# Optimization experiments

Measured on AMD Instinct MI355X. Metric: run time of the kernel, lower is better.

## Reference

```python
import jax, jax.numpy as jnp
import numpy as np

B, K, H, W = 8, 32, 480, 480
N, D = 576, 1024
NUM_CLASSES, CLS_DIM, OUT = 150, 64, 256
IN_DIM = D + CLS_DIM + 5


def setup_inputs() -> dict:
    key = jax.random.key(0)
    ks = jax.random.split(key, 8)
    return {
        "feature_map": jax.random.normal(ks[0], (B, N, D), dtype=jnp.float32),
        "masks": jax.random.randint(ks[1], (B, K, H, W), 0, 2, dtype=jnp.int32),
        "class_ids": jax.random.randint(ks[2], (B, K), 0, NUM_CLASSES, dtype=jnp.int64),
        "embed_table": jax.random.normal(ks[3], (NUM_CLASSES, CLS_DIM), dtype=jnp.float32),
        "W1": jax.random.normal(ks[4], (IN_DIM, OUT), dtype=jnp.float32) * 0.02,
        "b1": jnp.zeros((OUT,), dtype=jnp.float32),
        "ln_g": jnp.ones((OUT,), dtype=jnp.float32),
        "ln_b": jnp.zeros((OUT,), dtype=jnp.float32),
        "W2": jax.random.normal(ks[5], (OUT, OUT), dtype=jnp.float32) * 0.02,
        "b2": jnp.zeros((OUT,), dtype=jnp.float32),
    }


def _geom_feats(m):
    # m: [B,K,H,W] float binary masks -> [B,K,5] (cx, cy, area_norm, bbox_w, bbox_h)
    dt = m.dtype
    area = m.sum((-2, -1))                      # [B,K]
    safe = jnp.maximum(area, 1.0)
    xs = jnp.arange(W, dtype=dt)
    ys = jnp.arange(H, dtype=dt)
    cx = jnp.einsum('bkhw,w->bk', m, xs) / safe / W
    cy = jnp.einsum('bkhw,h->bk', m, ys) / safe / H
    col = m.max(axis=2)                          # [B,K,W] column occupancy
    row = m.max(axis=3)                          # [B,K,H] row occupancy
    x_min = jnp.min(jnp.where(col > 0, xs, float(W)), axis=-1)
    x_max = jnp.max(jnp.where(col > 0, xs, -1.0), axis=-1)
    y_min = jnp.min(jnp.where(row > 0, ys, float(H)), axis=-1)
    y_max = jnp.max(jnp.where(row > 0, ys, -1.0), axis=-1)
    bbox_w = (x_max - x_min + 1.0) / W
    bbox_h = (y_max - y_min + 1.0) / H
    area_norm = area / (H * W)
    geom = jnp.stack([cx, cy, area_norm, bbox_w, bbox_h], axis=-1)  # [B,K,5]
    valid = (area >= 1.0)[..., None]
    return jnp.where(valid, geom, 0.0)


def reference(feature_map, masks, class_ids, embed_table, W1, b1, ln_g, ln_b, W2, b2):
    Hf = Wf = int(round(N ** 0.5))  # 24
    m = (masks > 0).astype(feature_map.dtype)           # [B,K,H,W]
    # nearest-neighbor downsample (PyTorch 'nearest': src = floor(dst*in/out))
    idx_h = (jnp.arange(Hf) * H) // Hf
    idx_w = (jnp.arange(Wf) * W) // Wf
    m_rs = m[:, :, idx_h][:, :, :, idx_w]               # [B,K,Hf,Wf]
    m_flat = m_rs.reshape(B, K, Hf * Wf)                # [B,K,N]
    msum = jnp.clip(m_flat.sum(-1, keepdims=True), 1e-6, None)
    pooled = jnp.einsum('bkn,bnd->bkd', m_flat, feature_map) / msum  # [B,K,D]
    geom = _geom_feats(m)                               # [B,K,5]
    cls_emb = embed_table[class_ids]                    # [B,K,CLS_DIM]
    x = jnp.concatenate([pooled, cls_emb, geom], axis=-1)  # [B,K,IN_DIM]
    h = jax.nn.gelu(x @ W1 + b1, approximate=False)
    mu = h.mean(-1, keepdims=True)
    var = jnp.mean((h - mu) ** 2, axis=-1, keepdims=True)
    hn = (h - mu) * jax.lax.rsqrt(var + 1e-5) * ln_g + ln_b
    return hn @ W2 + b2                                 # [B,K,OUT]
```

## Files before the change

### kernel.cpp

```cpp
#include <hip/hip_runtime.h>
#include <math.h>

#define Bb 8
#define Kk 32
#define Hh 480
#define Ww 480
#define Nn 576
#define Dd 1024
#define CLSD 64
#define OUTD 256
#define INDIM 1093
#define BK 256
#define PIX4 57600

#define DS_OFF   0
#define META_OFF 147456

__global__ __launch_bounds__(1024) void kA(const int* __restrict__ masks,
                                           float* __restrict__ ws) {
  const int bk = blockIdx.x;
  const int t  = threadIdx.x;
  const int4* mp = (const int4*)(masks + (size_t)bk * (Hh * Ww));

  __shared__ float ds[576];
  __shared__ int s_area, s_sumx, s_sumy, s_cnt;
  __shared__ int s_minx, s_maxx, s_miny, s_maxy;
  if (t == 0) {
    s_area = 0; s_sumx = 0; s_sumy = 0; s_cnt = 0;
    s_minx = Ww; s_maxx = -1; s_miny = Hh; s_maxy = -1;
  }
  __syncthreads();

  int area = 0, sumx = 0, sumy = 0, cntds = 0;
  int minx = Ww, maxx = -1, miny = Hh, maxy = -1;

  auto body = [&](int q, int4 v) {
    int h   = q / 120;
    int rem = q - h * 120;
    int w0  = rem * 4;
    int m0 = v.x > 0, m1 = v.y > 0, m2 = v.z > 0, m3 = v.w > 0;
    int c = m0 + m1 + m2 + m3;
    area += c;
    sumy += h * c;
    sumx += w0 * c + m1 + 2 * m2 + 3 * m3;
    if (c) {
      miny = min(miny, h);
      maxy = max(maxy, h);
      int lo = m0 ? w0 : (m1 ? w0 + 1 : (m2 ? w0 + 2 : w0 + 3));
      int hi = m3 ? w0 + 3 : (m2 ? w0 + 2 : (m1 ? w0 + 1 : w0));
      minx = min(minx, lo);
      maxx = max(maxx, hi);
    }
    int a20 = h / 20;
    int c5  = rem / 5;
    if (h == a20 * 20 && rem == c5 * 5) {
      ds[a20 * 24 + c5] = (float)m0;
      cntds += m0;
    }
  };

#pragma unroll 4
  for (int i = 0; i < 56; i++) {
    int q = t + (i << 10);
    body(q, mp[q]);
  }
  if (t < 256) {
    int q = 57344 + t;
    body(q, mp[q]);
  }

  for (int off = 32; off; off >>= 1) {
    area  += __shfl_down(area, off);
    sumx  += __shfl_down(sumx, off);
    sumy  += __shfl_down(sumy, off);
    cntds += __shfl_down(cntds, off);
    minx = min(minx, __shfl_down(minx, off));
    maxx = max(maxx, __shfl_down(maxx, off));
    miny = min(miny, __shfl_down(miny, off));
    maxy = max(maxy, __shfl_down(maxy, off));
  }
  if ((t & 63) == 0) {
    atomicAdd(&s_area, area);
    atomicAdd(&s_sumx, sumx);
    atomicAdd(&s_sumy, sumy);
    atomicAdd(&s_cnt, cntds);
    atomicMin(&s_minx, minx);
    atomicMax(&s_maxx, maxx);
    atomicMin(&s_miny, miny);
    atomicMax(&s_maxy, maxy);
  }
  __syncthreads();

  float* ws_ds = ws + DS_OFF + (size_t)bk * 576;
  if (t < 576) ws_ds[t] = ds[t];

  if (t == 0) {
    float* meta = ws + META_OFF + (size_t)bk * 8;
    float areaf = (float)s_area;
    float safe  = fmaxf(areaf, 1.0f);
    float cx = ((float)s_sumx / safe) * (1.0f / Ww);
    float cy = ((float)s_sumy / safe) * (1.0f / Hh);
    float an = areaf * (1.0f / (Hh * Ww));
    float bw = (float)(s_maxx - s_minx + 1) * (1.0f / Ww);
    float bh = (float)(s_maxy - s_miny + 1) * (1.0f / Hh);
    if (s_area < 1) { cx = 0.f; cy = 0.f; an = 0.f; bw = 0.f; bh = 0.f; }
    meta[0] = cx; meta[1] = cy; meta[2] = an; meta[3] = bw; meta[4] = bh;
    meta[5] = 1.0f / fmaxf((float)s_cnt, 1e-6f);
    meta[6] = (float)s_cnt;
  }
}

__global__ __launch_bounds__(256) void kBC(const float* __restrict__ fm,
                                           const int* __restrict__ cids,
                                           const float* __restrict__ emb,
                                           const float* __restrict__ W1,
                                           const float* __restrict__ b1,
                                           const float* __restrict__ lg,
                                           const float* __restrict__ lb,
                                           const float* __restrict__ W2,
                                           const float* __restrict__ b2,
                                           const float* __restrict__ ws,
                                           float* __restrict__ out) {
  const int b    = blockIdx.x & 7;
  const int k    = blockIdx.x >> 3;
  const int bk   = b * Kk + k;
  const int t    = threadIdx.x;
  const int lane = t & 63;
  const int w    = t >> 6;

  __shared__ float4 x4s[292];
  __shared__ int   act[576];
  __shared__ int   nact;
  __shared__ float partial[4 * 256];
  __shared__ float hrow[256];
  __shared__ float red[8];
  float* x = (float*)x4s;

  if (t == 0) nact = 0;
  __syncthreads();

  const float* dsrow = ws + DS_OFF + (size_t)bk * 576;
  for (int i = t; i < 576; i += 256) {
    float mv = dsrow[i];
    if (mv != 0.0f) act[atomicAdd(&nact, 1)] = i;
  }
  if (t < 75) x[1093 + t] = 0.0f;
  __syncthreads();
  const int na = nact;

  const float* meta = ws + META_OFF + (size_t)bk * 8;
  float inv = meta[5];
  float ax = 0.f, ay = 0.f, az = 0.f, aw = 0.f;
  const float4* fmp = (const float4*)fm + (size_t)b * Nn * (Dd / 4);
  int j = 0;
  for (; j + 4 <= na; j += 4) {
    int4 nn = *(const int4*)(act + j);
    float4 f0 = fmp[nn.x * (Dd / 4) + t];
    float4 f1 = fmp[nn.y * (Dd / 4) + t];
    float4 f2 = fmp[nn.z * (Dd / 4) + t];
    float4 f3 = fmp[nn.w * (Dd / 4) + t];
    ax += f0.x + f1.x + f2.x + f3.x;
    ay += f0.y + f1.y + f2.y + f3.y;
    az += f0.z + f1.z + f2.z + f3.z;
    aw += f0.w + f1.w + f2.w + f3.w;
  }
  for (; j < na; j++) {
    float4 f = fmp[act[j] * (Dd / 4) + t];
    ax += f.x; ay += f.y; az += f.z; aw += f.w;
  }
  float4 p;
  p.x = ax * inv; p.y = ay * inv; p.z = az * inv; p.w = aw * inv;
  x4s[t] = p;
  if (t < CLSD) x[Dd + t] = emb[(size_t)cids[bk] * CLSD + t];
  else if (t < CLSD + 5) x[Dd + t] = meta[t - CLSD];
  __syncthreads();

  const int kbeg = w * 292;
  const int kend = min(INDIM, kbeg + 292);
  float acc0 = 0.f, acc1 = 0.f, acc2 = 0.f, acc3 = 0.f;
  int kk = kbeg;
  for (; kk + 4 <= kend; kk += 4) {
    float4 xv = x4s[kk >> 2];
    const float* xs = (const float*)&xv;
#pragma unroll
    for (int u = 0; u < 4; u++) {
      float xval = xs[u];
      const float* wrow = W1 + (size_t)(kk + u) * OUTD;
      acc0 = fmaf(xval, wrow[lane], acc0);
      acc1 = fmaf(xval, wrow[lane + 64], acc1);
      acc2 = fmaf(xval, wrow[lane + 128], acc2);
      acc3 = fmaf(xval, wrow[lane + 192], acc3);
    }
  }
  for (; kk < kend; kk++) {
    float xval = x[kk];
    const float* wrow = W1 + (size_t)kk * OUTD;
    acc0 = fmaf(xval, wrow[lane], acc0);
    acc1 = fmaf(xval, wrow[lane + 64], acc1);
    acc2 = fmaf(xval, wrow[lane + 128], acc2);
    acc3 = fmaf(xval, wrow[lane + 192], acc3);
  }
  partial[w * 256 + lane] = acc0;
  partial[w * 256 + lane + 64] = acc1;
  partial[w * 256 + lane + 128] = acc2;
  partial[w * 256 + lane + 192] = acc3;
  __syncthreads();

  float hval = partial[t] + partial[256 + t] + partial[512 + t] + partial[768 + t] + b1[t];
  hval = 0.5f * hval * (1.0f + erff(hval * 0.7071067811865475f));
  float s = hval, q = hval * hval;
  for (int off = 32; off; off >>= 1) {
    s += __shfl_down(s, off);
    q += __shfl_down(q, off);
  }
  if (lane == 0) { red[w] = s; red[4 + w] = q; }
  __syncthreads();
  float mu  = (red[0] + red[1] + red[2] + red[3]) * (1.0f / OUTD);
  float var = (red[4] + red[5] + red[6] + red[7]) * (1.0f / OUTD) - mu * mu;
  float ist = 1.0f / sqrtf(var + 1e-5f);
  float hn  = (hval - mu) * ist * lg[t] + lb[t];
  hrow[t] = hn;
  __syncthreads();

  float c = b2[t];
  const float4* h4 = (const float4*)hrow;
  for (int i = 0; i < 64; i++) {
    float4 hv = h4[i];
    const float* hs = (const float*)&hv;
#pragma unroll
    for (int u = 0; u < 4; u++)
      c = fmaf(hs[u], W2[(size_t)(i * 4 + u) * OUTD + t], c);
  }
  out[(size_t)bk * OUTD + t] = c;
}

extern "C" void kernel_launch(void* const* d_in, const int* in_sizes, int n_in,
                              void* d_out, int out_size, void* d_ws, size_t ws_size,
                              hipStream_t stream) {
  const float* fm    = (const float*)d_in[0];
  const int*   masks = (const int*)d_in[1];
  const int*   cids  = (const int*)d_in[2];
  const float* emb   = (const float*)d_in[3];
  const float* W1    = (const float*)d_in[4];
  const float* b1    = (const float*)d_in[5];
  const float* lg    = (const float*)d_in[6];
  const float* lb    = (const float*)d_in[7];
  const float* W2    = (const float*)d_in[8];
  const float* b2    = (const float*)d_in[9];
  float* out = (float*)d_out;
  float* ws  = (float*)d_ws;

  hipLaunchKernelGGL(kA, dim3(BK), dim3(1024), 0, stream, masks, ws);
  hipLaunchKernelGGL(kBC, dim3(BK), dim3(256), 0, stream, fm, cids, emb,
                     W1, b1, lg, lb, W2, b2, ws, out);
}
```

Baseline: 415.4 us.

## Fuse mask-geometry scan and pooled MLP into a single 1024-thread kernel

Merges the mask-scan kernel and the pooling/MLP kernel into one kernel. The downsampled mask and geometry metadata stay in shared memory instead of making a round trip through a global workspace, and one launch is removed. The feature gather and both GEMVs are also re-split across 16 waves using float4 weight loads, with the partial sums reduced in shared memory. In exchange, each block runs the MLP tail serially after its mask scan, and the larger shared-memory footprint could limit residency.

```diff
diff --git a/kernel.cpp b/kernel.cpp
--- a/kernel.cpp
+++ b/kernel.cpp
@@ -13,24 +13,44 @@
 #define BK 256
 #define PIX4 57600
 
-#define DS_OFF   0
-#define META_OFF 147456
-
-__global__ __launch_bounds__(1024) void kA(const int* __restrict__ masks,
-                                           float* __restrict__ ws) {
-  const int bk = blockIdx.x;
-  const int t  = threadIdx.x;
-  const int4* mp = (const int4*)(masks + (size_t)bk * (Hh * Ww));
-
-  __shared__ float ds[576];
+__global__ __launch_bounds__(1024) void kF(const int* __restrict__ masks,
+                                           const float* __restrict__ fm,
+                                           const int* __restrict__ cids,
+                                           const float* __restrict__ emb,
+                                           const float* __restrict__ W1,
+                                           const float* __restrict__ b1,
+                                           const float* __restrict__ lg,
+                                           const float* __restrict__ lb,
+                                           const float* __restrict__ W2,
+                                           const float* __restrict__ b2,
+                                           float* __restrict__ out) {
+  const int b    = blockIdx.x & 7;
+  const int k    = blockIdx.x >> 3;
+  const int bk   = b * Kk + k;
+  const int t    = threadIdx.x;
+  const int lane = t & 63;
+  const int w    = t >> 6;
+
+  __shared__ float  ds[576];
+  __shared__ int    act[576];
+  __shared__ float4 x4s[292];
+  __shared__ float4 pp[4 * 256];
+  __shared__ float  partial[16 * 256];
+  __shared__ float  hrow[256];
+  __shared__ float  red_s[16], red_q[16];
+  __shared__ float  gmeta[8];
   __shared__ int s_area, s_sumx, s_sumy, s_cnt;
-  __shared__ int s_minx, s_maxx, s_miny, s_maxy;
+  __shared__ int s_minx, s_maxx, s_miny, s_maxy, nact;
+  float* x = (float*)x4s;
+
   if (t == 0) {
     s_area = 0; s_sumx = 0; s_sumy = 0; s_cnt = 0;
     s_minx = Ww; s_maxx = -1; s_miny = Hh; s_maxy = -1;
-  }
-  __syncthreads();
-
+    nact = 0;
+  }
+  __syncthreads();
+
+  const int4* mp = (const int4*)(masks + (size_t)bk * (Hh * Ww));
   int area = 0, sumx = 0, sumy = 0, cntds = 0;
   int minx = Ww, maxx = -1, miny = Hh, maxy = -1;
 
@@ -79,7 +99,7 @@
     miny = min(miny, __shfl_down(miny, off));
     maxy = max(maxy, __shfl_down(maxy, off));
   }
-  if ((t & 63) == 0) {
+  if (lane == 0) {
     atomicAdd(&s_area, area);
     atomicAdd(&s_sumx, sumx);
     atomicAdd(&s_sumy, sumy);
@@ -91,11 +111,7 @@
   }
   __syncthreads();
 
-  float* ws_ds = ws + DS_OFF + (size_t)bk * 576;
-  if (t < 576) ws_ds[t] = ds[t];
-
   if (t == 0) {
-    float* meta = ws + META_OFF + (size_t)bk * 8;
     float areaf = (float)s_area;
     float safe  = fmaxf(areaf, 1.0f);
     float cx = ((float)s_sumx / safe) * (1.0f / Ww);
@@ -104,134 +120,140 @@
     float bw = (float)(s_maxx - s_minx + 1) * (1.0f / Ww);
     float bh = (float)(s_maxy - s_miny + 1) * (1.0f / Hh);
     if (s_area < 1) { cx = 0.f; cy = 0.f; an = 0.f; bw = 0.f; bh = 0.f; }
-    meta[0] = cx; meta[1] = cy; meta[2] = an; meta[3] = bw; meta[4] = bh;
-    meta[5] = 1.0f / fmaxf((float)s_cnt, 1e-6f);
-    meta[6] = (float)s_cnt;
-  }
-}
-
-__global__ __launch_bounds__(256) void kBC(const float* __restrict__ fm,
-                                           const int* __restrict__ cids,
-                                           const float* __restrict__ emb,
-                                           const float* __restrict__ W1,
-                                           const float* __restrict__ b1,
-                                           const float* __restrict__ lg,
-                                           const float* __restrict__ lb,
-                                           const float* __restrict__ W2,
-                                           const float* __restrict__ b2,
-                                           const float* __restrict__ ws,
-                                           float* __restrict__ out) {
-  const int b    = blockIdx.x & 7;
-  const int k    = blockIdx.x >> 3;
-  const int bk   = b * Kk + k;
-  const int t    = threadIdx.x;
-  const int lane = t & 63;
-  const int w    = t >> 6;
-
-  __shared__ float4 x4s[292];
-  __shared__ int   act[576];
-  __shared__ int   nact;
-  __shared__ float partial[4 * 256];
-  __shared__ float hrow[256];
-  __shared__ float red[8];
-  float* x = (float*)x4s;
-
-  if (t == 0) nact = 0;
-  __syncthreads();
-
-  const float* dsrow = ws + DS_OFF + (size_t)bk * 576;
-  for (int i = t; i < 576; i += 256) {
-    float mv = dsrow[i];
-    if (mv != 0.0f) act[atomicAdd(&nact, 1)] = i;
-  }
+    gmeta[0] = cx; gmeta[1] = cy; gmeta[2] = an; gmeta[3] = bw; gmeta[4] = bh;
+    gmeta[5] = 1.0f / fmaxf((float)s_cnt, 1e-6f);
+  }
+  if (t < 576 && ds[t] != 0.0f) act[atomicAdd(&nact, 1)] = t;
   if (t < 75) x[1093 + t] = 0.0f;
   __syncthreads();
   const int na = nact;
 
-  const float* meta = ws + META_OFF + (size_t)bk * 8;
-  float inv = meta[5];
-  float ax = 0.f, ay = 0.f, az = 0.f, aw = 0.f;
-  const float4* fmp = (const float4*)fm + (size_t)b * Nn * (Dd / 4);
-  int j = 0;
-  for (; j + 4 <= na; j += 4) {
-    int4 nn = *(const int4*)(act + j);
-    float4 f0 = fmp[nn.x * (Dd / 4) + t];
-    float4 f1 = fmp[nn.y * (Dd / 4) + t];
-    float4 f2 = fmp[nn.z * (Dd / 4) + t];
-    float4 f3 = fmp[nn.w * (Dd / 4) + t];
-    ax += f0.x + f1.x + f2.x + f3.x;
-    ay += f0.y + f1.y + f2.y + f3.y;
-    az += f0.z + f1.z + f2.z + f3.z;
-    aw += f0.w + f1.w + f2.w + f3.w;
-  }
-  for (; j < na; j++) {
-    float4 f = fmp[act[j] * (Dd / 4) + t];
-    ax += f.x; ay += f.y; az += f.z; aw += f.w;
-  }
-  float4 p;
-  p.x = ax * inv; p.y = ay * inv; p.z = az * inv; p.w = aw * inv;
-  x4s[t] = p;
-  if (t < CLSD) x[Dd + t] = emb[(size_t)cids[bk] * CLSD + t];
-  else if (t < CLSD + 5) x[Dd + t] = meta[t - CLSD];
-  __syncthreads();
-
-  const int kbeg = w * 292;
-  const int kend = min(INDIM, kbeg + 292);
-  float acc0 = 0.f, acc1 = 0.f, acc2 = 0.f, acc3 = 0.f;
-  int kk = kbeg;
-  for (; kk + 4 <= kend; kk += 4) {
-    float4 xv = x4s[kk >> 2];
-    const float* xs = (const float*)&xv;
-#pragma unroll
-    for (int u = 0; u < 4; u++) {
-      float xval = xs[u];
-      const float* wrow = W1 + (size_t)(kk + u) * OUTD;
-      acc0 = fmaf(xval, wrow[lane], acc0);
-      acc1 = fmaf(xval, wrow[lane + 64], acc1);
-      acc2 = fmaf(xval, wrow[lane + 128], acc2);
-      acc3 = fmaf(xval, wrow[lane + 192], acc3);
-    }
-  }
-  for (; kk < kend; kk++) {
-    float xval = x[kk];
-    const float* wrow = W1 + (size_t)kk * OUTD;
-    acc0 = fmaf(xval, wrow[lane], acc0);
-    acc1 = fmaf(xval, wrow[lane + 64], acc1);
-    acc2 = fmaf(xval, wrow[lane + 128], acc2);
-    acc3 = fmaf(xval, wrow[lane + 192], acc3);
-  }
-  partial[w * 256 + lane] = acc0;
-  partial[w * 256 + lane + 64] = acc1;
-  partial[w * 256 + lane + 128] = acc2;
-  partial[w * 256 + lane + 192] = acc3;
-  __syncthreads();
-
-  float hval = partial[t] + partial[256 + t] + partial[512 + t] + partial[768 + t] + b1[t];
-  hval = 0.5f * hval * (1.0f + erff(hval * 0.7071067811865475f));
-  float s = hval, q = hval * hval;
-  for (int off = 32; off; off >>= 1) {
-    s += __shfl_down(s, off);
-    q += __shfl_down(q, off);
-  }
-  if (lane == 0) { red[w] = s; red[4 + w] = q; }
-  __syncthreads();
-  float mu  = (red[0] + red[1] + red[2] + red[3]) * (1.0f / OUTD);
-  float var = (red[4] + red[5] + red[6] + red[7]) * (1.0f / OUTD) - mu * mu;
-  float ist = 1.0f / sqrtf(var + 1e-5f);
-  float hn  = (hval - mu) * ist * lg[t] + lb[t];
-  hrow[t] = hn;
-  __syncthreads();
-
-  float c = b2[t];
-  const float4* h4 = (const float4*)hrow;
-  for (int i = 0; i < 64; i++) {
-    float4 hv = h4[i];
-    const float* hs = (const float*)&hv;
-#pragma unroll
-    for (int u = 0; u < 4; u++)
-      c = fmaf(hs[u], W2[(size_t)(i * 4 + u) * OUTD + t], c);
-  }
-  out[(size_t)bk * OUTD + t] = c;
+  {
+    const int g   = t >> 8;
+    const int col = t & 255;
+    const int jb  = (na * g) >> 2;
+    const int je  = (na * (g + 1)) >> 2;
+    const float4* fmp = (const float4*)fm + (size_t)b * Nn * (Dd / 4);
+    float ax = 0.f, ay = 0.f, az = 0.f, aw = 0.f;
+    int j = jb;
+    for (; j + 4 <= je; j += 4) {
+      int n0 = act[j], n1 = act[j + 1], n2 = act[j + 2], n3 = act[j + 3];
+      float4 f0 = fmp[n0 * (Dd / 4) + col];
+      float4 f1 = fmp[n1 * (Dd / 4) + col];
+      float4 f2 = fmp[n2 * (Dd / 4) + col];
+      float4 f3 = fmp[n3 * (Dd / 4) + col];
+      ax += f0.x + f1.x + f2.x + f3.x;
+      ay += f0.y + f1.y + f2.y + f3.y;
+      az += f0.z + f1.z + f2.z + f3.z;
+      aw += f0.w + f1.w + f2.w + f3.w;
+    }
+    for (; j < je; j++) {
+      float4 f = fmp[act[j] * (Dd / 4) + col];
+      ax += f.x; ay += f.y; az += f.z; aw += f.w;
+    }
+    float4 p; p.x = ax; p.y = ay; p.z = az; p.w = aw;
+    pp[g * 256 + col] = p;
+  }
+  __syncthreads();
+
+  if (t < 256) {
+    float inv = gmeta[5];
+    float4 a0 = pp[t], a1 = pp[256 + t], a2 = pp[512 + t], a3 = pp[768 + t];
+    float4 p;
+    p.x = (a0.x + a1.x + a2.x + a3.x) * inv;
+    p.y = (a0.y + a1.y + a2.y + a3.y) * inv;
+    p.z = (a0.z + a1.z + a2.z + a3.z) * inv;
+    p.w = (a0.w + a1.w + a2.w + a3.w) * inv;
+    x4s[t] = p;
+  } else if (t < 320) {
+    x[Dd + (t - 256)] = emb[(size_t)cids[bk] * CLSD + (t - 256)];
+  } else if (t < 325) {
+    x[Dd + CLSD + (t - 320)] = gmeta[t - 320];
+  }
+  __syncthreads();
+
+  {
+    const int kbeg = w * 72;
+    const int kend = min(INDIM, kbeg + 72);
+    float4 acc = {0.f, 0.f, 0.f, 0.f};
+    int kk = kbeg;
+    for (; kk + 4 <= kend; kk += 4) {
+      float4 xv = x4s[kk >> 2];
+      const float* xs = (const float*)&xv;
+#pragma unroll
+      for (int u = 0; u < 4; u++) {
+        float4 w4 = *(const float4*)(W1 + (size_t)(kk + u) * OUTD + 4 * lane);
+        acc.x = fmaf(xs[u], w4.x, acc.x);
+        acc.y = fmaf(xs[u], w4.y, acc.y);
+        acc.z = fmaf(xs[u], w4.z, acc.z);
+        acc.w = fmaf(xs[u], w4.w, acc.w);
+      }
+    }
+    for (; kk < kend; kk++) {
+      float xv = x[kk];
+      float4 w4 = *(const float4*)(W1 + (size_t)kk * OUTD + 4 * lane);
+      acc.x = fmaf(xv, w4.x, acc.x);
+      acc.y = fmaf(xv, w4.y, acc.y);
+      acc.z = fmaf(xv, w4.z, acc.z);
+      acc.w = fmaf(xv, w4.w, acc.w);
+    }
+    *(float4*)(partial + w * 256 + 4 * lane) = acc;
+  }
+  __syncthreads();
+
+  float hv = 0.f;
+  if (t < 256) {
+    hv = b1[t];
+#pragma unroll
+    for (int ww = 0; ww < 16; ww++) hv += partial[ww * 256 + t];
+    hv = 0.5f * hv * (1.0f + erff(hv * 0.7071067811865475f));
+  }
+  {
+    float s = hv, q = hv * hv;
+    for (int off = 32; off; off >>= 1) {
+      s += __shfl_down(s, off);
+      q += __shfl_down(q, off);
+    }
+    if (lane == 0) { red_s[w] = s; red_q[w] = q; }
+  }
+  __syncthreads();
+  if (t < 256) {
+    float s = 0.f, q = 0.f;
+#pragma unroll
+    for (int ww = 0; ww < 16; ww++) { s += red_s[ww]; q += red_q[ww]; }
+    float mu  = s * (1.0f / OUTD);
+    float var = q * (1.0f / OUTD) - mu * mu;
+    float ist = 1.0f / sqrtf(var + 1e-5f);
+    hrow[t] = (hv - mu) * ist * lg[t] + lb[t];
+  }
+  __syncthreads();
+
+  {
+    float4 acc = {0.f, 0.f, 0.f, 0.f};
+#pragma unroll
+    for (int i = 0; i < 4; i++) {
+      float4 h4 = ((const float4*)hrow)[w * 4 + i];
+      const float* hs = (const float*)&h4;
+#pragma unroll
+      for (int u = 0; u < 4; u++) {
+        int kk = w * 16 + i * 4 + u;
+        float4 w4 = *(const float4*)(W2 + (size_t)kk * OUTD + 4 * lane);
+        acc.x = fmaf(hs[u], w4.x, acc.x);
+        acc.y = fmaf(hs[u], w4.y, acc.y);
+        acc.z = fmaf(hs[u], w4.z, acc.z);
+        acc.w = fmaf(hs[u], w4.w, acc.w);
+      }
+    }
+    *(float4*)(partial + w * 256 + 4 * lane) = acc;
+  }
+  __syncthreads();
+
+  if (t < 256) {
+    float c = b2[t];
+#pragma unroll
+    for (int ww = 0; ww < 16; ww++) c += partial[ww * 256 + t];
+    out[(size_t)bk * OUTD + t] = c;
+  }
 }
 
 extern "C" void kernel_launch(void* const* d_in, const int* in_sizes, int n_in,
@@ -248,9 +270,7 @@
   const float* W2    = (const float*)d_in[8];
   const float* b2    = (const float*)d_in[9];
   float* out = (float*)d_out;
-  float* ws  = (float*)d_ws;
-
-  hipLaunchKernelGGL(kA, dim3(BK), dim3(1024), 0, stream, masks, ws);
-  hipLaunchKernelGGL(kBC, dim3(BK), dim3(256), 0, stream, fm, cids, emb,
-                     W1, b1, lg, lb, W2, b2, ws, out);
+
+  hipLaunchKernelGGL(kF, dim3(BK), dim3(1024), 0, stream, masks, fm, cids, emb,
+                     W1, b1, lg, lb, W2, b2, out);
 }
```

Measured after the change: 374.5 us. 9.8% less time.
